# Kernel optimization log

Hardware: AMD Instinct MI355X
Metric: run time of the kernel (lower is better)

Reference implementation:

```python
import jax, jax.numpy as jnp
import numpy as np

NUM_WORDS = 32768
MAX_CHARS = 20
NUM_CHARS = 128
EMB = 64
H = 128   # word_hidden_size (per direction)
C = 128   # context_vector_size


def setup_inputs() -> dict:
    key = jax.random.key(0)
    ks = jax.random.split(key, 16)
    s = 1.0 / np.sqrt(H)  # torch GRU default init scale
    u = lambda k, shape, sc: jax.random.uniform(k, shape, jnp.float32, -sc, sc)
    inp = {
        'padded_char_tensor': jax.random.randint(ks[0], (NUM_WORDS, MAX_CHARS), 0, NUM_CHARS),
        'sequence_lens': jax.random.randint(ks[1], (NUM_WORDS,), 1, MAX_CHARS + 1),
        'emb': jax.random.normal(ks[2], (NUM_CHARS, EMB), jnp.float32),
        # forward-direction GRU params (torch layout: gates r,z,n stacked)
        'Wih_f': u(ks[3], (3 * H, EMB), s),
        'Whh_f': u(ks[4], (3 * H, H), s),
        'bih_f': u(ks[5], (3 * H,), s),
        'bhh_f': u(ks[6], (3 * H,), s),
        # backward-direction GRU params
        'Wih_b': u(ks[7], (3 * H, EMB), s),
        'Whh_b': u(ks[8], (3 * H, H), s),
        'bih_b': u(ks[9], (3 * H,), s),
        'bhh_b': u(ks[10], (3 * H,), s),
        # word_projection Linear(2H -> C)
        'Wp': u(ks[11], (C, 2 * H), 1.0 / np.sqrt(2 * H)),
        'bp': u(ks[12], (C,), 1.0 / np.sqrt(2 * H)),
        # word context vector [C, 1]
        'ctx': u(ks[13], (C, 1), 0.1),
    }
    return inp


def _gru_dir(x_proj, Whh, bhh):
    # x_proj: [B, T, 3H] precomputed input projection; scan over T
    Hn = Whh.shape[1]
    def step(h, xt):
        hp = h @ Whh.T + bhh
        r = jax.nn.sigmoid(xt[:, :Hn] + hp[:, :Hn])
        z = jax.nn.sigmoid(xt[:, Hn:2 * Hn] + hp[:, Hn:2 * Hn])
        n = jnp.tanh(xt[:, 2 * Hn:] + r * hp[:, 2 * Hn:])
        h = (1.0 - z) * n + z * h
        return h, h
    h0 = jnp.zeros((x_proj.shape[0], Hn), x_proj.dtype)
    _, ys = jax.lax.scan(step, h0, x_proj.transpose(1, 0, 2))
    return ys.transpose(1, 0, 2)  # [B, T, H]


def _rev_within(x, lens):
    # reverse each sequence within its valid length (packed-sequence semantics)
    T = x.shape[1]
    t = jnp.arange(T)[None, :]
    idx = jnp.where(t < lens[:, None], lens[:, None] - 1 - t, t)
    return jnp.take_along_axis(x, idx[:, :, None], axis=1)


def _forward(chars, lens, emb, Wih_f, Whh_f, bih_f, bhh_f,
             Wih_b, Whh_b, bih_b, bhh_b, Wp, bp, ctx):
    x = emb[chars]  # [B, T, EMB]; dropout_p=0 -> identity
    mask = (jnp.arange(x.shape[1])[None, :] < lens[:, None])  # [B, T]
    out_f = _gru_dir(x @ Wih_f.T + bih_f, Whh_f, bhh_f)
    xb = _rev_within(x, lens)
    out_b = _gru_dir(xb @ Wih_b.T + bih_b, Whh_b, bhh_b)
    out_b = _rev_within(out_b, lens)
    # pad_packed_sequence zero-pads beyond each length
    out = jnp.concatenate([out_f, out_b], axis=-1) * mask[:, :, None]  # [B, T, 2H]
    proj = jnp.tanh(out @ Wp.T + bp)                # [B, T, C]
    scores = jnp.einsum('btc,c->bt', proj, ctx[:, 0])
    att = jax.nn.softmax(scores, axis=-1)           # softmax over char positions
    return jnp.einsum('bt,btd->bd', att, out)       # [B, 2H]


def reference(padded_char_tensor, sequence_lens, emb, Wih_f, Whh_f, bih_f, bhh_f,
              Wih_b, Whh_b, bih_b, bhh_b, Wp, bp, ctx):
    return _forward(padded_char_tensor, sequence_lens, emb, Wih_f, Whh_f, bih_f,
                    bhh_f, Wih_b, Whh_b, bih_b, bhh_b, Wp, bp, ctx)
```

## Files before the change

kernel.cpp:

```cpp
#include <hip/hip_runtime.h>
#include <hip/hip_bf16.h>
#include <stdint.h>


typedef unsigned short u16;
typedef float f32x4 __attribute__((ext_vector_type(4)));
typedef __bf16 bf16x8 __attribute__((ext_vector_type(8)));

#if __has_builtin(__builtin_amdgcn_exp2f)
#define EXP2F(x) __builtin_amdgcn_exp2f(x)
#else
#define EXP2F(x) exp2f(x)
#endif
#if __has_builtin(__builtin_amdgcn_rcpf)
#define RCPF(x) __builtin_amdgcn_rcpf(x)
#else
#define RCPF(x) (1.0f / (x))
#endif

#define LOG2E 1.4426950408889634f

__device__ __forceinline__ u16 f2b(float f) {
  uint32_t u = __builtin_bit_cast(uint32_t, f);
  u = u + 0x7FFFu + ((u >> 16) & 1u);
  return (u16)(u >> 16);
}
__device__ __forceinline__ float b2f(u16 s) {
  uint32_t u = ((uint32_t)s) << 16;
  return __builtin_bit_cast(float, u);
}
__device__ __forceinline__ float fast_sig(float x) {
  return RCPF(1.0f + EXP2F(-LOG2E * x));
}
__device__ __forceinline__ float fast_tanh(float x) {
  return 1.0f - 2.0f * RCPF(EXP2F(2.0f * LOG2E * x) + 1.0f);
}

__global__ void prep_kernel(
    const float* __restrict__ emb,
    const float* __restrict__ wih_f, const float* __restrict__ bih_f,
    const float* __restrict__ wih_b, const float* __restrict__ bih_b,
    const float* __restrict__ whh_f_in, const float* __restrict__ whh_b_in,
    const float* __restrict__ wp_in,
    u16* __restrict__ xpb_f, u16* __restrict__ xpb_b,
    u16* __restrict__ whhf, u16* __restrict__ whhb, u16* __restrict__ wpf) {
  int gid = blockIdx.x * 256 + threadIdx.x;
  if (blockIdx.x < 512) {
    int d = gid >> 16;
    int r = gid & 65535;
    int c = r >> 9;
    int r2 = r & 511;
    int wc = r2 >> 3;
    int i8 = r2 & 7;
    float v = 0.f;
    if (i8 < 6) {
      int cls = i8 >> 1, j2 = i8 & 1;
      int gate = cls * 128 + (wc >> 4) * 32 + j2 * 16 + (wc & 15);
      const float* wih = d ? wih_b : wih_f;
      const float* bih = d ? bih_b : bih_f;
      const float4* e4 = (const float4*)(emb + c * 64);
      const float4* w4 = (const float4*)(wih + gate * 64);
      float s = 0.f;
#pragma unroll
      for (int e = 0; e < 16; e++) {
        float4 a = e4[e], b = w4[e];
        s += a.x * b.x + a.y * b.y + a.z * b.z + a.w * b.w;
      }
      v = s + bih[gate];
    }
    (d ? xpb_b : xpb_f)[(c << 9) + r2] = f2b(v);
  } else if (blockIdx.x < 560) {
    int idx = gid - 512 * 256;
    int d = (idx >= 6144) ? 1 : 0;
    int r = idx - d * 6144;
    int lane = r & 63, kt = (r >> 6) & 3, nt = r >> 8;
    int n = nt * 16 + (lane & 15);
    int k0 = kt * 32 + (lane >> 4) * 8;
    const float* w = d ? whh_b_in : whh_f_in;
    u16* o = (d ? whhb : whhf) + r * 8;
    for (int j = 0; j < 8; j++) o[j] = f2b(w[n * 128 + k0 + j]);
  } else {
    int idx = gid - 560 * 256;
    if (idx < 4096) {
      int lane = idx & 63, kt = (idx >> 6) & 7, nt = idx >> 9;
      int n = nt * 16 + (lane & 15);
      int k0 = kt * 32 + (lane >> 4) * 8;
      u16* o = wpf + idx * 8;
      for (int j = 0; j < 8; j++) o[j] = f2b(wp_in[n * 256 + k0 + j]);
    }
  }
}

__global__ void sort_zero(int* __restrict__ bins) {
  if (threadIdx.x < 32) bins[threadIdx.x] = 0;
}
__global__ void sort_hist(const int* __restrict__ lens, int* __restrict__ bins) {
  __shared__ int hcnt[32];
  int tid = threadIdx.x;
  if (tid < 32) hcnt[tid] = 0;
  __syncthreads();
  int gid = blockIdx.x * 256 + tid;
  int l = lens[gid] & 31;
  atomicAdd(&hcnt[l], 1);
  __syncthreads();
  if (tid < 32 && hcnt[tid]) atomicAdd(&bins[tid], hcnt[tid]);
}
__global__ void sort_scan(const int* __restrict__ bins, int* __restrict__ offsw,
                          const float* __restrict__ bp,
                          const float* __restrict__ ctx,
                          float* __restrict__ c0out) {
  if (threadIdx.x == 0 && blockIdx.x == 0) {
    int off = 0;
    for (int l = 0; l < 32; l++) {
      offsw[l] = off;
      off += bins[l];
    }
    float c0 = 0.f;
    for (int c = 0; c < 128; c++) c0 += fast_tanh(bp[c]) * ctx[c];
    *c0out = c0;
  }
}
__global__ void sort_scat(const int* __restrict__ lens, int* __restrict__ offsw,
                          int* __restrict__ perm) {
  __shared__ int lcnt[32];
  __shared__ int lbase[32];
  int tid = threadIdx.x;
  if (tid < 32) lcnt[tid] = 0;
  __syncthreads();
  int gid = blockIdx.x * 256 + tid;
  int l = lens[gid] & 31;
  int lr = atomicAdd(&lcnt[l], 1);
  __syncthreads();
  if (tid < 32) lbase[tid] = lcnt[tid] ? atomicAdd(&offsw[tid], lcnt[tid]) : 0;
  __syncthreads();
  perm[lbase[l] + lr] = gid;
}

__global__ __launch_bounds__(256, 1) void gru_kernel(
    const int* __restrict__ chars, const int* __restrict__ lens,
    const int* __restrict__ perm,
    const u16* __restrict__ xpb_f, const u16* __restrict__ xpb_b,
    const u16* __restrict__ whhf, const u16* __restrict__ whhb,
    const float* __restrict__ bhh_f, const float* __restrict__ bhh_b,
    u16* __restrict__ hf, u16* __restrict__ hb, int word_off) {
  const int bid = blockIdx.x;
  const int dir = bid & 1;
  const int wg = bid >> 1;
  const int tid = threadIdx.x;

  __shared__ int perm_s[16];
  __shared__ unsigned char lens_s[16];
  __shared__ unsigned char chars_s[320];
  __shared__ u16 h_s[2][2048];

  if (tid < 16) {
    int p = perm[word_off + wg * 16 + tid];
    perm_s[tid] = p;
    lens_s[tid] = (unsigned char)lens[p];
  }
  for (int i = tid; i < 1024; i += 256) ((uint32_t*)h_s[0])[i] = 0u;
  __syncthreads();

  for (int i = tid; i < 320; i += 256) {
    int w = i & 15, s = i >> 4;
    int L = lens_s[w];
    int t = dir ? ((s < L) ? (L - 1 - s) : s) : s;
    chars_s[s * 16 + w] = (unsigned char)chars[perm_s[w] * 20 + t];
  }

  const u16* xp = dir ? xpb_b : xpb_f;
  const u16* whh = dir ? whhb : whhf;
  const float* bhh = dir ? bhh_b : bhh_f;
  u16* hout = (dir ? hb : hf) + (size_t)wg * 16 * 2560;

  const int wv = tid >> 6, ln = tid & 63, col = ln & 15, grp = ln >> 4;

  bf16x8 Bf[6][4];
#pragma unroll
  for (int n = 0; n < 6; n++) {
    int cls = n >> 1, j2 = n & 1;
    int nt = cls * 8 + wv * 2 + j2;
#pragma unroll
    for (int kt = 0; kt < 4; kt++)
      Bf[n][kt] = *(const bf16x8*)(whh + (((nt * 4 + kt) * 64 + ln) << 3));
  }

  float bh[6];
#pragma unroll
  for (int n = 0; n < 6; n++) {
    int cls = n >> 1, j2 = n & 1;
    bh[n] = bhh[cls * 128 + wv * 32 + j2 * 16 + col];
  }

  __syncthreads();

  int Lmax = 1;
  for (int i = 0; i < 16; i++) Lmax = max(Lmax, (int)lens_s[i]);

  const int swd = tid >> 4;
  const int k16 = (tid & 15) << 3;
  const int skt = k16 >> 5;
  const int slan = swd | (((k16 >> 3) & 3) << 4);
  const int sL = lens_s[swd];

  float h[4][2];
#pragma unroll
  for (int r = 0; r < 4; r++) { h[r][0] = 0.f; h[r][1] = 0.f; }

  for (int s = 0; s < Lmax; s++) {
    const u16* hcur = h_s[s & 1];
    u16* hnxt = h_s[(s + 1) & 1];

    uint4 xq[4];
#pragma unroll
    for (int r = 0; r < 4; r++) {
      int c = chars_s[s * 16 + grp * 4 + r];
      xq[r] = *(const uint4*)(xp + (((c << 6) + (wv << 4) + col) << 3));
    }

    f32x4 acc[6];
#pragma unroll
    for (int n = 0; n < 6; n++) acc[n] = (f32x4){bh[n], bh[n], bh[n], bh[n]};
#pragma unroll
    for (int kt = 0; kt < 4; kt++) {
      bf16x8 Af = *(const bf16x8*)(hcur + ((kt * 64 + ln) << 3));
#pragma unroll
      for (int n = 0; n < 6; n++)
        acc[n] = __builtin_amdgcn_mfma_f32_16x16x32_bf16(Af, Bf[n][kt], acc[n], 0, 0, 0);
    }

#pragma unroll
    for (int r = 0; r < 4; r++) {
      const u16* e = (const u16*)&xq[r];
#pragma unroll
      for (int j2 = 0; j2 < 2; j2++) {
        float rr = fast_sig(b2f(e[j2]) + acc[j2][r]);
        float zz = fast_sig(b2f(e[2 + j2]) + acc[2 + j2][r]);
        float nn = fast_tanh(b2f(e[4 + j2]) + rr * acc[4 + j2][r]);
        float hn = (1.f - zz) * nn + zz * h[r][j2];
        h[r][j2] = hn;
        int lane_a = (grp * 4 + r) | ((j2 * 2 + (col >> 3)) << 4);
        hnxt[((wv * 64 + lane_a) << 3) + (col & 7)] = f2b(hn);
      }
    }
    __syncthreads();

    if (s < sL) {
      int tdst = dir ? (sL - 1 - s) : s;
      uint4 v = *(const uint4*)(hnxt + ((skt * 64 + slan) << 3));
      *(uint4*)(hout + ((size_t)swd * 20 + tdst) * 128 + k16) = v;
    }
  }
}

__global__ __launch_bounds__(256, 2) void attn_kernel(
    const u16* __restrict__ hf, const u16* __restrict__ hb,
    const u16* __restrict__ wpf,
    const float* __restrict__ bp, const float* __restrict__ ctx,
    const int* __restrict__ perm, const int* __restrict__ lens,
    const float* __restrict__ c0p,
    float* __restrict__ out, int word_off) {
  const int blk = blockIdx.x;
  const int lw0 = blk * 16;

  __shared__ u16 ot_s[4096];
  __shared__ float part_s[4][16];
  __shared__ int perm_s[16];
  __shared__ unsigned char lens_s[16];

  const int tid = threadIdx.x;
  const int wv = tid >> 6, ln = tid & 63, col = ln & 15, grp = ln >> 4;
  const int sw = tid >> 4;
  const int seg = tid & 15;

  if (tid < 16) {
    int p = perm[word_off + lw0 + tid];
    perm_s[tid] = p;
    lens_s[tid] = (unsigned char)lens[p];
  }
  __syncthreads();
  int Lmax = 1;
#pragma unroll
  for (int i = 0; i < 16; i++) Lmax = max(Lmax, (int)lens_s[i]);
  const int Lw = lens_s[sw];

  float bpv[2], ctxv[2];
#pragma unroll
  for (int n = 0; n < 2; n++) {
    int nt = wv + n * 4;
    bpv[n] = bp[nt * 16 + col];
    ctxv[n] = ctx[nt * 16 + col];
  }

  float facc[16];
#pragma unroll
  for (int i = 0; i < 16; i++) facc[i] = 0.f;
  float mrun = -3.0e38f, drun = 0.f;

  const u16* srcbase =
      ((seg < 8) ? hf : hb) + (size_t)(lw0 + sw) * 2560 + (seg & 7) * 16;

  uint4 vn[2];
#pragma unroll
  for (int q = 0; q < 2; q++) vn[q] = *(const uint4*)(srcbase + q * 8);

  for (int t = 0; t < Lmax; t++) {
    uint4 v[2];
    v[0] = vn[0];
    v[1] = vn[1];

#pragma unroll
    for (int q = 0; q < 2; q++) {
      int idx = seg * 2 + q;
      int kt = idx >> 2;
      int lane_a = sw | ((idx & 3) << 4);
      *(uint4*)(ot_s + ((kt * 64 + lane_a) << 3)) = v[q];
    }
    if (t + 1 < Lmax) {
      const u16* src = srcbase + (t + 1) * 128;
#pragma unroll
      for (int q = 0; q < 2; q++) vn[q] = *(const uint4*)(src + q * 8);
    }
    __syncthreads();

    f32x4 acc[2];
#pragma unroll
    for (int n = 0; n < 2; n++) acc[n] = (f32x4){bpv[n], bpv[n], bpv[n], bpv[n]};

#pragma unroll
    for (int kt = 0; kt < 8; kt++) {
      bf16x8 Af = *(const bf16x8*)(ot_s + ((kt * 64 + ln) << 3));
#pragma unroll
      for (int n = 0; n < 2; n++) {
        int nt = wv + n * 4;
        bf16x8 Bf = *(const bf16x8*)(wpf + (((nt * 8 + kt) * 64 + ln) << 3));
        acc[n] = __builtin_amdgcn_mfma_f32_16x16x32_bf16(Af, Bf, acc[n], 0, 0, 0);
      }
    }

#pragma unroll
    for (int r = 0; r < 4; r++) {
      float p = fast_tanh(acc[0][r]) * ctxv[0] + fast_tanh(acc[1][r]) * ctxv[1];
      p += __shfl_xor(p, 1, 64);
      p += __shfl_xor(p, 2, 64);
      p += __shfl_xor(p, 4, 64);
      p += __shfl_xor(p, 8, 64);
      if (col == 0) part_s[wv][grp * 4 + r] = p;
    }
    __syncthreads();

    float sc = part_s[0][sw] + part_s[1][sw] + part_s[2][sw] + part_s[3][sw];

    if (t < Lw) {
      float mnew = fmaxf(mrun, sc);
      float scale = EXP2F(LOG2E * (mrun - mnew));
      float e = EXP2F(LOG2E * (sc - mnew));
      drun = drun * scale + e;
      mrun = mnew;
#pragma unroll
      for (int q = 0; q < 2; q++) {
        const u16* pv = (const u16*)&v[q];
#pragma unroll
        for (int j = 0; j < 8; j++)
          facc[q * 8 + j] = facc[q * 8 + j] * scale + e * b2f(pv[j]);
      }
    }
  }

  drun += (float)(20 - Lw) * EXP2F(LOG2E * (*c0p - mrun));

  float inv = RCPF(drun);
  float* dst = out + (size_t)perm_s[sw] * 256 + seg * 16;
#pragma unroll
  for (int i = 0; i < 4; i++) {
    float4 o = make_float4(facc[i * 4] * inv, facc[i * 4 + 1] * inv,
                           facc[i * 4 + 2] * inv, facc[i * 4 + 3] * inv);
    *(float4*)(dst + i * 4) = o;
  }
}

extern "C" void kernel_launch(void* const* d_in, const int* in_sizes, int n_in,
                              void* d_out, int out_size, void* d_ws, size_t ws_size,
                              hipStream_t stream) {
  const int* chars = (const int*)d_in[0];
  const int* lens = (const int*)d_in[1];
  const float* emb = (const float*)d_in[2];
  const float* wih_f = (const float*)d_in[3];
  const float* whh_f = (const float*)d_in[4];
  const float* bih_f = (const float*)d_in[5];
  const float* bhh_f = (const float*)d_in[6];
  const float* wih_b = (const float*)d_in[7];
  const float* whh_b = (const float*)d_in[8];
  const float* bih_b = (const float*)d_in[9];
  const float* bhh_b = (const float*)d_in[10];
  const float* wp = (const float*)d_in[11];
  const float* bp = (const float*)d_in[12];
  const float* ctx = (const float*)d_in[13];
  float* outp = (float*)d_out;

  uint8_t* ws = (uint8_t*)d_ws;
  u16* xpb_f = (u16*)(ws + 0);
  u16* xpb_b = (u16*)(ws + 131072);
  u16* whhf = (u16*)(ws + 262144);
  u16* whhb = (u16*)(ws + 360448);
  u16* wpf = (u16*)(ws + 458752);
  int* bins = (int*)(ws + 524288);
  int* offsw = (int*)(ws + 524416);
  float* c0p = (float*)(ws + 524544);
  int* permp = (int*)(ws + 524560);
  const size_t H_OFF = 786432;

  prep_kernel<<<576, 256, 0, stream>>>(emb, wih_f, bih_f, wih_b, bih_b, whh_f,
                                       whh_b, wp, xpb_f, xpb_b, whhf, whhb, wpf);
  sort_zero<<<1, 64, 0, stream>>>(bins);
  sort_hist<<<128, 256, 0, stream>>>(lens, bins);
  sort_scan<<<1, 64, 0, stream>>>(bins, offsw, bp, ctx, c0p);
  sort_scat<<<128, 256, 0, stream>>>(lens, offsw, permp);

  const size_t per_word = 20 * 128 * 2 * 2;
  size_t avail = (ws_size > H_OFF) ? (ws_size - H_OFF) : 0;
  int maxw = (int)(avail / per_word) & ~63;
  if (maxw > 32768) maxw = 32768;
  if (maxw < 64) maxw = 64;

  for (int done = 0; done < 32768;) {
    int nw = (32768 - done < maxw) ? (32768 - done) : maxw;
    u16* hfp = (u16*)(ws + H_OFF);
    u16* hbp = hfp + (size_t)nw * 2560;
    gru_kernel<<<(nw / 16) * 2, 256, 0, stream>>>(
        chars, lens, permp, xpb_f, xpb_b, whhf, whhb, bhh_f, bhh_b, hfp, hbp, done);
    attn_kernel<<<nw / 16, 256, 0, stream>>>(hfp, hbp, wpf, bp, ctx, permp,
                                             lens, c0p, outp, done);
    done += nw;
  }
}
```

Before: 269.7 us.

## Split GRU gate columns across 8 waves, prefetch input projections, reverse block order

The GRU kernel grows from 256 to 512 threads. Each wave now handles one 16-column half of the gate outputs (3 MFMA tiles instead of 6), which halves per-wave serial MFMA and activation work on the recurrent critical path. The input-projection table is re-laid out so each lane loads a compact uint2, and the next step's projection is prefetched a step ahead. Blocks are processed in reverse sorted order so the longest words start first, and Lmax is read from the last sorted entry instead of computed with a loop. The costs are higher register and LDS-sync pressure per block and a larger workspace.

```diff
diff --git a/kernel.cpp b/kernel.cpp
--- a/kernel.cpp
+++ b/kernel.cpp
@@ -42,20 +42,21 @@
     const float* __restrict__ wih_b, const float* __restrict__ bih_b,
     const float* __restrict__ whh_f_in, const float* __restrict__ whh_b_in,
     const float* __restrict__ wp_in,
-    u16* __restrict__ xpb_f, u16* __restrict__ xpb_b,
+    u16* __restrict__ xpj_f, u16* __restrict__ xpj_b,
     u16* __restrict__ whhf, u16* __restrict__ whhb, u16* __restrict__ wpf) {
   int gid = blockIdx.x * 256 + threadIdx.x;
-  if (blockIdx.x < 512) {
-    int d = gid >> 16;
-    int r = gid & 65535;
-    int c = r >> 9;
-    int r2 = r & 511;
-    int wc = r2 >> 3;
-    int i8 = r2 & 7;
+  if (blockIdx.x < 1024) {
+    int d = gid >> 17;
+    int r = gid & 131071;
+    int c = r >> 10;
+    int r2 = r & 1023;
+    int j2 = r2 >> 9;
+    int r3 = r2 & 511;
+    int w16 = r3 >> 2;
+    int slot = r3 & 3;
     float v = 0.f;
-    if (i8 < 6) {
-      int cls = i8 >> 1, j2 = i8 & 1;
-      int gate = cls * 128 + (wc >> 4) * 32 + j2 * 16 + (wc & 15);
+    if (slot < 3) {
+      int gate = slot * 128 + (w16 >> 4) * 32 + j2 * 16 + (w16 & 15);
       const float* wih = d ? wih_b : wih_f;
       const float* bih = d ? bih_b : bih_f;
       const float4* e4 = (const float4*)(emb + c * 64);
@@ -68,9 +69,9 @@
       }
       v = s + bih[gate];
     }
-    (d ? xpb_b : xpb_f)[(c << 9) + r2] = f2b(v);
-  } else if (blockIdx.x < 560) {
-    int idx = gid - 512 * 256;
+    (d ? xpj_b : xpj_f)[r] = f2b(v);
+  } else if (blockIdx.x < 1072) {
+    int idx = gid - 1024 * 256;
     int d = (idx >= 6144) ? 1 : 0;
     int r = idx - d * 6144;
     int lane = r & 63, kt = (r >> 6) & 3, nt = r >> 8;
@@ -80,7 +81,7 @@
     u16* o = (d ? whhb : whhf) + r * 8;
     for (int j = 0; j < 8; j++) o[j] = f2b(w[n * 128 + k0 + j]);
   } else {
-    int idx = gid - 560 * 256;
+    int idx = gid - 1072 * 256;
     if (idx < 4096) {
       int lane = idx & 63, kt = (idx >> 6) & 7, nt = idx >> 9;
       int n = nt * 16 + (lane & 15);
@@ -136,16 +137,16 @@
   perm[lbase[l] + lr] = gid;
 }
 
-__global__ __launch_bounds__(256, 1) void gru_kernel(
+__global__ __launch_bounds__(512, 4) void gru_kernel(
     const int* __restrict__ chars, const int* __restrict__ lens,
     const int* __restrict__ perm,
-    const u16* __restrict__ xpb_f, const u16* __restrict__ xpb_b,
+    const u16* __restrict__ xpj_f, const u16* __restrict__ xpj_b,
     const u16* __restrict__ whhf, const u16* __restrict__ whhb,
     const float* __restrict__ bhh_f, const float* __restrict__ bhh_b,
-    u16* __restrict__ hf, u16* __restrict__ hb, int word_off) {
+    u16* __restrict__ hf, u16* __restrict__ hb, int word_off, int nbd) {
   const int bid = blockIdx.x;
   const int dir = bid & 1;
-  const int wg = bid >> 1;
+  const int wg = nbd - 1 - (bid >> 1);
   const int tid = threadIdx.x;
 
   __shared__ int perm_s[16];
@@ -158,97 +159,104 @@
     perm_s[tid] = p;
     lens_s[tid] = (unsigned char)lens[p];
   }
-  for (int i = tid; i < 1024; i += 256) ((uint32_t*)h_s[0])[i] = 0u;
-  __syncthreads();
-
-  for (int i = tid; i < 320; i += 256) {
+  for (int i = tid; i < 1024; i += 512) ((uint32_t*)h_s[0])[i] = 0u;
+  __syncthreads();
+
+  for (int i = tid; i < 320; i += 512) {
     int w = i & 15, s = i >> 4;
     int L = lens_s[w];
     int t = dir ? ((s < L) ? (L - 1 - s) : s) : s;
     chars_s[s * 16 + w] = (unsigned char)chars[perm_s[w] * 20 + t];
   }
 
-  const u16* xp = dir ? xpb_b : xpb_f;
+  const u16* xp = dir ? xpj_b : xpj_f;
   const u16* whh = dir ? whhb : whhf;
   const float* bhh = dir ? bhh_b : bhh_f;
   u16* hout = (dir ? hb : hf) + (size_t)wg * 16 * 2560;
 
   const int wv = tid >> 6, ln = tid & 63, col = ln & 15, grp = ln >> 4;
-
-  bf16x8 Bf[6][4];
-#pragma unroll
-  for (int n = 0; n < 6; n++) {
-    int cls = n >> 1, j2 = n & 1;
-    int nt = cls * 8 + wv * 2 + j2;
+  const int j2 = wv & 1, hg = wv >> 1;
+
+  bf16x8 Bf[3][4];
+#pragma unroll
+  for (int cls = 0; cls < 3; cls++) {
+    int nt = cls * 8 + hg * 2 + j2;
 #pragma unroll
     for (int kt = 0; kt < 4; kt++)
-      Bf[n][kt] = *(const bf16x8*)(whh + (((nt * 4 + kt) * 64 + ln) << 3));
-  }
-
-  float bh[6];
-#pragma unroll
-  for (int n = 0; n < 6; n++) {
-    int cls = n >> 1, j2 = n & 1;
-    bh[n] = bhh[cls * 128 + wv * 32 + j2 * 16 + col];
-  }
-
-  __syncthreads();
-
-  int Lmax = 1;
-  for (int i = 0; i < 16; i++) Lmax = max(Lmax, (int)lens_s[i]);
-
-  const int swd = tid >> 4;
-  const int k16 = (tid & 15) << 3;
-  const int skt = k16 >> 5;
-  const int slan = swd | (((k16 >> 3) & 3) << 4);
+      Bf[cls][kt] = *(const bf16x8*)(whh + (((nt * 4 + kt) * 64 + ln) << 3));
+  }
+
+  float bh[3];
+#pragma unroll
+  for (int cls = 0; cls < 3; cls++)
+    bh[cls] = bhh[cls * 128 + hg * 32 + j2 * 16 + col];
+
+  __syncthreads();
+
+  const int Lmax = lens_s[15];
+
+  const int swd = tid >> 5;
+  const int k4 = (tid & 31) << 2;
+  const int skt = k4 >> 5;
+  const int slan = swd | (((k4 >> 3) & 3) << 4);
+  const int sslot = k4 & 7;
   const int sL = lens_s[swd];
 
-  float h[4][2];
-#pragma unroll
-  for (int r = 0; r < 4; r++) { h[r][0] = 0.f; h[r][1] = 0.f; }
+  float h[4] = {0.f, 0.f, 0.f, 0.f};
+
+  uint2 xq[4];
+#pragma unroll
+  for (int r = 0; r < 4; r++) {
+    int c = chars_s[grp * 4 + r];
+    xq[r] = *(const uint2*)(xp + ((((c << 1) + j2) << 7) + (hg << 4) + col) * 4);
+  }
 
   for (int s = 0; s < Lmax; s++) {
     const u16* hcur = h_s[s & 1];
     u16* hnxt = h_s[(s + 1) & 1];
 
-    uint4 xq[4];
-#pragma unroll
-    for (int r = 0; r < 4; r++) {
-      int c = chars_s[s * 16 + grp * 4 + r];
-      xq[r] = *(const uint4*)(xp + (((c << 6) + (wv << 4) + col) << 3));
-    }
-
-    f32x4 acc[6];
-#pragma unroll
-    for (int n = 0; n < 6; n++) acc[n] = (f32x4){bh[n], bh[n], bh[n], bh[n]};
+    uint2 xc[4];
+#pragma unroll
+    for (int r = 0; r < 4; r++) xc[r] = xq[r];
+    if (s + 1 < Lmax) {
+#pragma unroll
+      for (int r = 0; r < 4; r++) {
+        int c = chars_s[(s + 1) * 16 + grp * 4 + r];
+        xq[r] =
+            *(const uint2*)(xp + ((((c << 1) + j2) << 7) + (hg << 4) + col) * 4);
+      }
+    }
+
+    f32x4 acc[3];
+#pragma unroll
+    for (int cls = 0; cls < 3; cls++)
+      acc[cls] = (f32x4){bh[cls], bh[cls], bh[cls], bh[cls]};
 #pragma unroll
     for (int kt = 0; kt < 4; kt++) {
       bf16x8 Af = *(const bf16x8*)(hcur + ((kt * 64 + ln) << 3));
 #pragma unroll
-      for (int n = 0; n < 6; n++)
-        acc[n] = __builtin_amdgcn_mfma_f32_16x16x32_bf16(Af, Bf[n][kt], acc[n], 0, 0, 0);
+      for (int cls = 0; cls < 3; cls++)
+        acc[cls] =
+            __builtin_amdgcn_mfma_f32_16x16x32_bf16(Af, Bf[cls][kt], acc[cls], 0, 0, 0);
     }
 
 #pragma unroll
     for (int r = 0; r < 4; r++) {
-      const u16* e = (const u16*)&xq[r];
-#pragma unroll
-      for (int j2 = 0; j2 < 2; j2++) {
-        float rr = fast_sig(b2f(e[j2]) + acc[j2][r]);
-        float zz = fast_sig(b2f(e[2 + j2]) + acc[2 + j2][r]);
-        float nn = fast_tanh(b2f(e[4 + j2]) + rr * acc[4 + j2][r]);
-        float hn = (1.f - zz) * nn + zz * h[r][j2];
-        h[r][j2] = hn;
-        int lane_a = (grp * 4 + r) | ((j2 * 2 + (col >> 3)) << 4);
-        hnxt[((wv * 64 + lane_a) << 3) + (col & 7)] = f2b(hn);
-      }
+      const u16* e = (const u16*)&xc[r];
+      float rr = fast_sig(b2f(e[0]) + acc[0][r]);
+      float zz = fast_sig(b2f(e[1]) + acc[1][r]);
+      float nn = fast_tanh(b2f(e[2]) + rr * acc[2][r]);
+      float hn = (1.f - zz) * nn + zz * h[r];
+      h[r] = hn;
+      int lane_a = (grp * 4 + r) | ((j2 * 2 + (col >> 3)) << 4);
+      hnxt[((hg * 64 + lane_a) << 3) + (col & 7)] = f2b(hn);
     }
     __syncthreads();
 
     if (s < sL) {
       int tdst = dir ? (sL - 1 - s) : s;
-      uint4 v = *(const uint4*)(hnxt + ((skt * 64 + slan) << 3));
-      *(uint4*)(hout + ((size_t)swd * 20 + tdst) * 128 + k16) = v;
+      uint2 v = *(const uint2*)(hnxt + ((skt * 64 + slan) << 3) + sslot);
+      *(uint2*)(hout + ((size_t)swd * 20 + tdst) * 128 + k4) = v;
     }
   }
 }
@@ -260,7 +268,7 @@
     const int* __restrict__ perm, const int* __restrict__ lens,
     const float* __restrict__ c0p,
     float* __restrict__ out, int word_off) {
-  const int blk = blockIdx.x;
+  const int blk = gridDim.x - 1 - blockIdx.x;
   const int lw0 = blk * 16;
 
   __shared__ u16 ot_s[4096];
@@ -279,9 +287,7 @@
     lens_s[tid] = (unsigned char)lens[p];
   }
   __syncthreads();
-  int Lmax = 1;
-#pragma unroll
-  for (int i = 0; i < 16; i++) Lmax = max(Lmax, (int)lens_s[i]);
+  const int Lmax = lens_s[15];
   const int Lw = lens_s[sw];
 
   float bpv[2], ctxv[2];
@@ -399,19 +405,19 @@
   float* outp = (float*)d_out;
 
   uint8_t* ws = (uint8_t*)d_ws;
-  u16* xpb_f = (u16*)(ws + 0);
-  u16* xpb_b = (u16*)(ws + 131072);
-  u16* whhf = (u16*)(ws + 262144);
-  u16* whhb = (u16*)(ws + 360448);
-  u16* wpf = (u16*)(ws + 458752);
-  int* bins = (int*)(ws + 524288);
-  int* offsw = (int*)(ws + 524416);
-  float* c0p = (float*)(ws + 524544);
-  int* permp = (int*)(ws + 524560);
-  const size_t H_OFF = 786432;
-
-  prep_kernel<<<576, 256, 0, stream>>>(emb, wih_f, bih_f, wih_b, bih_b, whh_f,
-                                       whh_b, wp, xpb_f, xpb_b, whhf, whhb, wpf);
+  u16* xpj_f = (u16*)(ws + 0);
+  u16* xpj_b = (u16*)(ws + 262144);
+  u16* whhf = (u16*)(ws + 524288);
+  u16* whhb = (u16*)(ws + 622592);
+  u16* wpf = (u16*)(ws + 720896);
+  int* bins = (int*)(ws + 786432);
+  int* offsw = (int*)(ws + 786560);
+  float* c0p = (float*)(ws + 786688);
+  int* permp = (int*)(ws + 786752);
+  const size_t H_OFF = 1048576;
+
+  prep_kernel<<<1088, 256, 0, stream>>>(emb, wih_f, bih_f, wih_b, bih_b, whh_f,
+                                        whh_b, wp, xpj_f, xpj_b, whhf, whhb, wpf);
   sort_zero<<<1, 64, 0, stream>>>(bins);
   sort_hist<<<128, 256, 0, stream>>>(lens, bins);
   sort_scan<<<1, 64, 0, stream>>>(bins, offsw, bp, ctx, c0p);
@@ -427,8 +433,10 @@
     int nw = (32768 - done < maxw) ? (32768 - done) : maxw;
     u16* hfp = (u16*)(ws + H_OFF);
     u16* hbp = hfp + (size_t)nw * 2560;
-    gru_kernel<<<(nw / 16) * 2, 256, 0, stream>>>(
-        chars, lens, permp, xpb_f, xpb_b, whhf, whhb, bhh_f, bhh_b, hfp, hbp, done);
+    int nbd = nw / 16;
+    gru_kernel<<<2 * nbd, 512, 0, stream>>>(chars, lens, permp, xpj_f, xpj_b,
+                                            whhf, whhb, bhh_f, bhh_b, hfp, hbp,
+                                            done, nbd);
     attn_kernel<<<nw / 16, 256, 0, stream>>>(hfp, hbp, wpf, bp, ctx, permp,
                                              lens, c0p, outp, done);
     done += nw;
```

After: 262.8 us (median of 2 runs). -2.5%, faster.
